# Optimization experiments

Measured on AMD Instinct MI355X. Metric: run time of the kernel, lower is better.

## Reference

```python
import jax, jax.numpy as jnp
import numpy as np

FILTER_SIZE = 7
SIGMA = 1.5
K1 = 0.01
K2 = 0.03
MAX_VAL = 1.0
CHANNEL = 1


def _gaussian_kernel3d(size, channel, sigma):
    coords = jnp.arange(size, dtype=jnp.float32) - (size - 1.0) / 2.0
    g = -(coords ** 2) / (2.0 * sigma ** 2)
    # grid[i,j,k] = g[j] + g[i] + g[k], matching torch view(1,-1,1)+view(-1,1,1)+view(1,1,-1)
    grid = g[None, :, None] + g[:, None, None] + g[None, None, :]
    grid = jax.nn.softmax(grid.reshape(-1))
    kernel = grid.reshape(1, 1, size, size, size)
    return jnp.broadcast_to(kernel, (channel, 1, size, size, size))


def _dwconv3d(x, kernel, channel):
    # depthwise (groups=channel) valid conv, NCDHW
    return jax.lax.conv_general_dilated(
        x, kernel, window_strides=(1, 1, 1), padding='VALID',
        dimension_numbers=('NCDHW', 'OIDHW', 'NCDHW'),
        feature_group_count=channel)


def setup_inputs() -> dict:
    key = jax.random.key(0)
    k1, k2 = jax.random.split(key)
    shape = (2, 1, 192, 192, 192)
    return {
        'input': jax.random.uniform(k1, shape, dtype=jnp.float32),
        'target': jax.random.uniform(k2, shape, dtype=jnp.float32),
    }


def reference(input, target):
    kernel = _gaussian_kernel3d(FILTER_SIZE, CHANNEL, SIGMA)
    c1 = (K1 * MAX_VAL) ** 2
    c2 = (K2 * MAX_VAL) ** 2
    mu1 = _dwconv3d(input, kernel, CHANNEL)
    mu2 = _dwconv3d(target, kernel, CHANNEL)
    mu1_sq = mu1 * mu1
    mu2_sq = mu2 * mu2
    mu1_mu2 = mu1 * mu2
    sigma1_sq = _dwconv3d(input * input, kernel, CHANNEL) - mu1_sq
    sigma2_sq = _dwconv3d(target * target, kernel, CHANNEL) - mu2_sq
    sigma12 = _dwconv3d(input * target, kernel, CHANNEL) - mu1_mu2
    v1 = 2.0 * sigma12 + c2
    v2 = sigma1_sq + sigma2_sq + c2
    ssim = (2.0 * mu1_mu2 + c1) * v1 / ((mu1_sq + mu2_sq + c1) * v2)
    return jnp.mean(ssim)  # reduction='mean'
```

## Files before the change

### kernel.cpp

```cpp
#include <hip/hip_runtime.h>
#include <utility>


#define DIMS 192
#define OD   186
#define VOL  (DIMS * DIMS * DIMS)
#define ZCH  62
#define XCH  27
#define NCHX 7
#define NP   (XCH + 6)
#define YT   8
#define YIN  14

#define ZP_P   15
#define ZP_F   (ZCH * ZP_P)
#define YP_F   576
#define YP_OFF (5 * ZP_F)
#define LDS_N  (YP_OFF + 5 * YP_F)

__global__ __launch_bounds__(256, 4)
void ssim3d_kernel(const float* __restrict__ X, const float* __restrict__ Y,
                   double* __restrict__ acc_out) {
    __shared__ float lds[LDS_N];
    __shared__ float wsum[4];
    const int tid = threadIdx.x;

    float w[7];
    {
        float s = 0.f;
        #pragma unroll
        for (int t = 0; t < 7; ++t) {
            float d = (float)t - 3.0f;
            w[t] = expf(-d * d / 4.5f);
            s += w[t];
        }
        #pragma unroll
        for (int t = 0; t < 7; ++t)
            w[t] = __uint_as_float(__builtin_amdgcn_readfirstlane(__float_as_uint(w[t] / s)));
    }

    const int z0 = blockIdx.x * ZCH;
    const int y0 = blockIdx.y * YT;
    const int cx = blockIdx.z % NCHX;
    const int n  = blockIdx.z / NCHX;
    const int x0 = cx * XCH;

    const float* Xb = X + (size_t)n * VOL;
    const float* Yb = Y + (size_t)n * VOL;

    const int zj = tid >> 4;
    const int zs = tid & 15;
    const bool zact = (zj < YIN);
    const int zc = z0 + zs * 4;
    const int gy = min(y0 + zj, DIMS - 1);
    const unsigned rowoff = (unsigned)gy * DIMS + (unsigned)zc;
    const bool ztail = (zc + 9 > DIMS - 1);

    const int wv = tid >> 6;
    const int ln = tid & 63;
    const int ybase = (310 * wv) >> 2;
    const int ycnt  = ((310 * (wv + 1)) >> 2) - ybase;

    const int aj = wv;
    const int ak = ln;
    const bool v1 = (ak < ZCH) && (y0 + aj < OD);
    const bool v2 = (ak < ZCH) && (y0 + aj + 4 < OD);
    const int xmax = OD + 6 - x0;

    float acc[7][10];
    #pragma unroll
    for (int q = 0; q < 7; ++q)
        #pragma unroll
        for (int m = 0; m < 10; ++m) acc[q][m] = 0.f;

    float lsum = 0.f;
    const float c1 = 1e-4f, c2 = 9e-4f;

    float pfx[10], pfy[10];

    auto loadX = [&](int xi) {
        if (!zact) return;
        int gx = min(x0 + xi, DIMS - 1);
        const float* p = Xb + (size_t)gx * (DIMS * DIMS) + rowoff;
        #pragma unroll
        for (int t = 0; t < 4; ++t) {
            float2 a = *(const float2*)(p + 2 * t);
            pfx[2 * t] = a.x; pfx[2 * t + 1] = a.y;
        }
        if (!ztail) {
            float2 a = *(const float2*)(p + 8);
            pfx[8] = a.x; pfx[9] = a.y;
        } else { pfx[8] = 0.f; pfx[9] = 0.f; }
    };
    auto loadY = [&](int xi) {
        if (!zact) return;
        int gx = min(x0 + xi, DIMS - 1);
        const float* p = Yb + (size_t)gx * (DIMS * DIMS) + rowoff;
        #pragma unroll
        for (int t = 0; t < 4; ++t) {
            float2 a = *(const float2*)(p + 2 * t);
            pfy[2 * t] = a.x; pfy[2 * t + 1] = a.y;
        }
        if (!ztail) {
            float2 a = *(const float2*)(p + 8);
            pfy[8] = a.x; pfy[9] = a.y;
        } else { pfy[8] = 0.f; pfy[9] = 0.f; }
    };

    auto ssim_pt = [&](float mu1, float mu2, float ex2, float ey2, float exy) {
        float mu11 = mu1 * mu1, mu22 = mu2 * mu2, mu12 = mu1 * mu2;
        float num = (2.f * mu12 + c1) * (2.f * (exy - mu12) + c2);
        float den = (mu11 + mu22 + c1) * ((ex2 - mu11) + (ey2 - mu22) + c2);
        lsum += num * __builtin_amdgcn_rcpf(den);
    };

    auto body = [&](int xi, auto ucell) {
        constexpr int U = decltype(ucell)::value;

        if (zact) {
            #pragma unroll
            for (int o = 0; o < 4; ++o) {
                float a0 = 0.f, a1 = 0.f, a2 = 0.f, a3 = 0.f, a4 = 0.f;
                #pragma unroll
                for (int t = 0; t < 7; ++t) {
                    float xx = pfx[o + t], yy = pfy[o + t], wt = w[t];
                    a0 += wt * xx;
                    a1 += wt * yy;
                    a2 += wt * (xx * xx);
                    a3 += wt * (yy * yy);
                    a4 += wt * (xx * yy);
                }
                int k = zs * 4 + o;
                if (k < ZCH) {
                    int b = k * ZP_P + zj;
                    lds[b]            = a0;
                    lds[b + ZP_F]     = a1;
                    lds[b + 2 * ZP_F] = a2;
                    lds[b + 3 * ZP_F] = a3;
                    lds[b + 4 * ZP_F] = a4;
                }
            }
        }
        if (xi + 1 < NP) loadX(xi + 1);
        __syncthreads();

        #pragma unroll
        for (int p2 = 0; p2 < 2; ++p2) {
            int rel = p2 * 64 + ln;
            if (rel < ycnt) {
                int t = ybase + rel;
                int f = t / ZCH;
                int k = t - f * ZCH;
                const float* src = &lds[f * ZP_F + k * ZP_P];
                float v[YIN];
                #pragma unroll
                for (int jj = 0; jj < YIN; ++jj) v[jj] = src[jj];
                float* dst = &lds[YP_OFF + f * YP_F + k * 9];
                #pragma unroll
                for (int j = 0; j < YT; ++j) {
                    float a = 0.f;
                    #pragma unroll
                    for (int tt = 0; tt < 7; ++tt) a += w[tt] * v[j + tt];
                    dst[j] = a;
                }
            }
        }
        if (xi + 1 < NP) loadY(xi + 1);
        __syncthreads();

        float vv[10];
        #pragma unroll
        for (int f = 0; f < 5; ++f) {
            vv[2 * f]     = lds[YP_OFF + f * YP_F + ak * 9 + aj];
            vv[2 * f + 1] = lds[YP_OFF + f * YP_F + ak * 9 + aj + 4];
        }
        #pragma unroll
        for (int d = 0; d < 7; ++d) {
            float wq = w[d];
            #pragma unroll
            for (int m = 0; m < 10; ++m)
                acc[(U + 7 - d) % 7][m] += wq * vv[m];
        }
        constexpr int sc = (U + 1) % 7;
        if (xi >= 6 && xi < xmax) {
            if (v1) ssim_pt(acc[sc][0], acc[sc][2], acc[sc][4], acc[sc][6], acc[sc][8]);
            if (v2) ssim_pt(acc[sc][1], acc[sc][3], acc[sc][5], acc[sc][7], acc[sc][9]);
        }
        #pragma unroll
        for (int m = 0; m < 10; ++m) acc[sc][m] = 0.f;
    };

    loadX(0); loadY(0);
    #pragma unroll 1
    for (int b = 0; b < 28; b += 7) {
        body(b + 0, std::integral_constant<int, 0>{});
        body(b + 1, std::integral_constant<int, 1>{});
        body(b + 2, std::integral_constant<int, 2>{});
        body(b + 3, std::integral_constant<int, 3>{});
        body(b + 4, std::integral_constant<int, 4>{});
        body(b + 5, std::integral_constant<int, 5>{});
        body(b + 6, std::integral_constant<int, 6>{});
    }
    body(28, std::integral_constant<int, 0>{});
    body(29, std::integral_constant<int, 1>{});
    body(30, std::integral_constant<int, 2>{});
    body(31, std::integral_constant<int, 3>{});
    body(32, std::integral_constant<int, 4>{});

    #pragma unroll
    for (int off = 32; off > 0; off >>= 1) lsum += __shfl_down(lsum, off, 64);
    if ((tid & 63) == 0) wsum[tid >> 6] = lsum;
    __syncthreads();
    if (tid == 0)
        atomicAdd(acc_out, (double)(wsum[0] + wsum[1] + wsum[2] + wsum[3]));
}

__global__ void ssim3d_finalize(const double* __restrict__ acc, float* __restrict__ out) {
    out[0] = (float)(acc[0] / 12869712.0);
}

extern "C" void kernel_launch(void* const* d_in, const int* in_sizes, int n_in,
                              void* d_out, int out_size, void* d_ws, size_t ws_size,
                              hipStream_t stream) {
    (void)in_sizes; (void)n_in; (void)out_size; (void)ws_size;
    const float* x = (const float*)d_in[0];
    const float* y = (const float*)d_in[1];
    float* out = (float*)d_out;
    double* acc = (double*)d_ws;
    hipMemsetAsync(d_ws, 0, sizeof(double), stream);
    dim3 grid(3, 24, NCHX * 2);
    ssim3d_kernel<<<grid, 256, 0, stream>>>(x, y, acc);
    ssim3d_finalize<<<1, 1, 0, stream>>>(acc, out);
}
```

Baseline: 237.8 us.

## Shrink z-tile, fuse y-pass into output stage, double-buffer LDS

The z chunk per block drops from 62 to 32, giving 6 z tiles and a larger grid, and occupancy is raised to 6 blocks per CU. The separate y-convolution pass through LDS is gone: each output thread now reads the 7 z-filtered rows directly and applies the y filter inline. The LDS tile is double-buffered so one barrier per x-step is enough, and X and Y prefetches are issued together. The global double atomic is replaced by per-block partial slots reduced by a 256-thread finalize kernel, when workspace allows. In exchange there is more redundant y-halo work per block and more LDS reads per output point.

```diff
diff --git a/kernel.cpp b/kernel.cpp
--- a/kernel.cpp
+++ b/kernel.cpp
@@ -5,22 +5,23 @@
 #define DIMS 192
 #define OD   186
 #define VOL  (DIMS * DIMS * DIMS)
-#define ZCH  62
+#define ZCH  32
+#define NZT  6
 #define XCH  27
 #define NCHX 7
 #define NP   (XCH + 6)
 #define YT   8
 #define YIN  14
-
-#define ZP_P   15
-#define ZP_F   (ZCH * ZP_P)
-#define YP_F   576
-#define YP_OFF (5 * ZP_F)
-#define LDS_N  (YP_OFF + 5 * YP_F)
-
-__global__ __launch_bounds__(256, 4)
+#define NBLK (NZT * 24 * NCHX * 2)
+
+#define ZP_J 34
+#define ZP_F (YIN * ZP_J)
+#define ZP_B (5 * ZP_F)
+#define LDS_N (2 * ZP_B)
+
+__global__ __launch_bounds__(256, 6)
 void ssim3d_kernel(const float* __restrict__ X, const float* __restrict__ Y,
-                   double* __restrict__ acc_out) {
+                   double* __restrict__ part, int use_slots) {
     __shared__ float lds[LDS_N];
     __shared__ float wsum[4];
     const int tid = threadIdx.x;
@@ -51,184 +52,179 @@
     const int zj = tid >> 4;
     const int zs = tid & 15;
     const bool zact = (zj < YIN);
-    const int zc = z0 + zs * 4;
     const int gy = min(y0 + zj, DIMS - 1);
-    const unsigned rowoff = (unsigned)gy * DIMS + (unsigned)zc;
-    const bool ztail = (zc + 9 > DIMS - 1);
-
-    const int wv = tid >> 6;
-    const int ln = tid & 63;
-    const int ybase = (310 * wv) >> 2;
-    const int ycnt  = ((310 * (wv + 1)) >> 2) - ybase;
-
-    const int aj = wv;
-    const int ak = ln;
-    const bool v1 = (ak < ZCH) && (y0 + aj < OD);
-    const bool v2 = (ak < ZCH) && (y0 + aj + 4 < OD);
-    const int xmax = OD + 6 - x0;
-
-    float acc[7][10];
+    const int zbase = z0 + 2 * zs;
+    const bool ztail = (zbase + 7 > DIMS - 1);
+    const unsigned rowoff = (unsigned)gy * DIMS + (unsigned)zbase;
+
+    const int cj = tid >> 5;
+    const int ck = tid & 31;
+    const bool cvalid = (z0 + ck < OD) && (y0 + cj < OD);
+    const int xmax = DIMS - x0;
+
+    float acc[7][5];
     #pragma unroll
     for (int q = 0; q < 7; ++q)
         #pragma unroll
-        for (int m = 0; m < 10; ++m) acc[q][m] = 0.f;
+        for (int m = 0; m < 5; ++m) acc[q][m] = 0.f;
 
     float lsum = 0.f;
     const float c1 = 1e-4f, c2 = 9e-4f;
 
-    float pfx[10], pfy[10];
+    float pfx[8], pfy[8];
 
     auto loadX = [&](int xi) {
         if (!zact) return;
         int gx = min(x0 + xi, DIMS - 1);
-        const float* p = Xb + (size_t)gx * (DIMS * DIMS) + rowoff;
-        #pragma unroll
-        for (int t = 0; t < 4; ++t) {
-            float2 a = *(const float2*)(p + 2 * t);
-            pfx[2 * t] = a.x; pfx[2 * t + 1] = a.y;
-        }
+        const float* p = Xb + (size_t)gx * (DIMS * DIMS);
         if (!ztail) {
-            float2 a = *(const float2*)(p + 8);
-            pfx[8] = a.x; pfx[9] = a.y;
-        } else { pfx[8] = 0.f; pfx[9] = 0.f; }
+            const float* q = p + rowoff;
+            #pragma unroll
+            for (int t = 0; t < 4; ++t) {
+                float2 a = *(const float2*)(q + 2 * t);
+                pfx[2 * t] = a.x; pfx[2 * t + 1] = a.y;
+            }
+        } else {
+            #pragma unroll
+            for (int t = 0; t < 8; ++t)
+                pfx[t] = p[(unsigned)gy * DIMS + (unsigned)min(zbase + t, DIMS - 1)];
+        }
     };
     auto loadY = [&](int xi) {
         if (!zact) return;
         int gx = min(x0 + xi, DIMS - 1);
-        const float* p = Yb + (size_t)gx * (DIMS * DIMS) + rowoff;
-        #pragma unroll
-        for (int t = 0; t < 4; ++t) {
-            float2 a = *(const float2*)(p + 2 * t);
-            pfy[2 * t] = a.x; pfy[2 * t + 1] = a.y;
-        }
+        const float* p = Yb + (size_t)gx * (DIMS * DIMS);
         if (!ztail) {
-            float2 a = *(const float2*)(p + 8);
-            pfy[8] = a.x; pfy[9] = a.y;
-        } else { pfy[8] = 0.f; pfy[9] = 0.f; }
+            const float* q = p + rowoff;
+            #pragma unroll
+            for (int t = 0; t < 4; ++t) {
+                float2 a = *(const float2*)(q + 2 * t);
+                pfy[2 * t] = a.x; pfy[2 * t + 1] = a.y;
+            }
+        } else {
+            #pragma unroll
+            for (int t = 0; t < 8; ++t)
+                pfy[t] = p[(unsigned)gy * DIMS + (unsigned)min(zbase + t, DIMS - 1)];
+        }
     };
 
-    auto ssim_pt = [&](float mu1, float mu2, float ex2, float ey2, float exy) {
-        float mu11 = mu1 * mu1, mu22 = mu2 * mu2, mu12 = mu1 * mu2;
-        float num = (2.f * mu12 + c1) * (2.f * (exy - mu12) + c2);
-        float den = (mu11 + mu22 + c1) * ((ex2 - mu11) + (ey2 - mu22) + c2);
-        lsum += num * __builtin_amdgcn_rcpf(den);
-    };
-
-    auto body = [&](int xi, auto ucell) {
-        constexpr int U = decltype(ucell)::value;
+    auto body = [&](int xi, auto uc, auto pc) {
+        constexpr int U = decltype(uc)::value;
+        constexpr int P = decltype(pc)::value;
+        constexpr int BUF = P * ZP_B;
 
         if (zact) {
-            #pragma unroll
-            for (int o = 0; o < 4; ++o) {
-                float a0 = 0.f, a1 = 0.f, a2 = 0.f, a3 = 0.f, a4 = 0.f;
+            float a0[2] = {0.f, 0.f}, a1[2] = {0.f, 0.f}, a2[2] = {0.f, 0.f},
+                  a3[2] = {0.f, 0.f}, a4[2] = {0.f, 0.f};
+            #pragma unroll
+            for (int t = 0; t < 7; ++t) {
+                float wt = w[t];
                 #pragma unroll
-                for (int t = 0; t < 7; ++t) {
-                    float xx = pfx[o + t], yy = pfy[o + t], wt = w[t];
-                    a0 += wt * xx;
-                    a1 += wt * yy;
-                    a2 += wt * (xx * xx);
-                    a3 += wt * (yy * yy);
-                    a4 += wt * (xx * yy);
-                }
-                int k = zs * 4 + o;
-                if (k < ZCH) {
-                    int b = k * ZP_P + zj;
-                    lds[b]            = a0;
-                    lds[b + ZP_F]     = a1;
-                    lds[b + 2 * ZP_F] = a2;
-                    lds[b + 3 * ZP_F] = a3;
-                    lds[b + 4 * ZP_F] = a4;
+                for (int o = 0; o < 2; ++o) {
+                    float xx = pfx[t + o], yy = pfy[t + o];
+                    a0[o] += wt * xx;
+                    a1[o] += wt * yy;
+                    a2[o] += wt * (xx * xx);
+                    a3[o] += wt * (yy * yy);
+                    a4[o] += wt * (xx * yy);
                 }
             }
-        }
-        if (xi + 1 < NP) loadX(xi + 1);
+            const int wb = BUF + zj * ZP_J + 2 * zs;
+            *(float2*)&lds[wb]            = make_float2(a0[0], a0[1]);
+            *(float2*)&lds[wb + ZP_F]     = make_float2(a1[0], a1[1]);
+            *(float2*)&lds[wb + 2 * ZP_F] = make_float2(a2[0], a2[1]);
+            *(float2*)&lds[wb + 3 * ZP_F] = make_float2(a3[0], a3[1]);
+            *(float2*)&lds[wb + 4 * ZP_F] = make_float2(a4[0], a4[1]);
+        }
+        if (xi + 1 < NP) { loadX(xi + 1); loadY(xi + 1); }
         __syncthreads();
 
-        #pragma unroll
-        for (int p2 = 0; p2 < 2; ++p2) {
-            int rel = p2 * 64 + ln;
-            if (rel < ycnt) {
-                int t = ybase + rel;
-                int f = t / ZCH;
-                int k = t - f * ZCH;
-                const float* src = &lds[f * ZP_F + k * ZP_P];
-                float v[YIN];
-                #pragma unroll
-                for (int jj = 0; jj < YIN; ++jj) v[jj] = src[jj];
-                float* dst = &lds[YP_OFF + f * YP_F + k * 9];
-                #pragma unroll
-                for (int j = 0; j < YT; ++j) {
-                    float a = 0.f;
-                    #pragma unroll
-                    for (int tt = 0; tt < 7; ++tt) a += w[tt] * v[j + tt];
-                    dst[j] = a;
-                }
-            }
-        }
-        if (xi + 1 < NP) loadY(xi + 1);
-        __syncthreads();
-
-        float vv[10];
+        const float* src = &lds[BUF + cj * ZP_J + ck];
+        float vv[5];
         #pragma unroll
         for (int f = 0; f < 5; ++f) {
-            vv[2 * f]     = lds[YP_OFF + f * YP_F + ak * 9 + aj];
-            vv[2 * f + 1] = lds[YP_OFF + f * YP_F + ak * 9 + aj + 4];
+            float a = 0.f;
+            #pragma unroll
+            for (int t = 0; t < 7; ++t) a += w[t] * src[f * ZP_F + t * ZP_J];
+            vv[f] = a;
         }
         #pragma unroll
         for (int d = 0; d < 7; ++d) {
             float wq = w[d];
             #pragma unroll
-            for (int m = 0; m < 10; ++m)
+            for (int m = 0; m < 5; ++m)
                 acc[(U + 7 - d) % 7][m] += wq * vv[m];
         }
         constexpr int sc = (U + 1) % 7;
-        if (xi >= 6 && xi < xmax) {
-            if (v1) ssim_pt(acc[sc][0], acc[sc][2], acc[sc][4], acc[sc][6], acc[sc][8]);
-            if (v2) ssim_pt(acc[sc][1], acc[sc][3], acc[sc][5], acc[sc][7], acc[sc][9]);
-        }
-        #pragma unroll
-        for (int m = 0; m < 10; ++m) acc[sc][m] = 0.f;
+        if (xi >= 6 && xi < xmax && cvalid) {
+            float mu1 = acc[sc][0], mu2 = acc[sc][1];
+            float ex2 = acc[sc][2], ey2 = acc[sc][3], exy = acc[sc][4];
+            float mu11 = mu1 * mu1, mu22 = mu2 * mu2, mu12 = mu1 * mu2;
+            float num = (2.f * mu12 + c1) * (2.f * (exy - mu12) + c2);
+            float den = (mu11 + mu22 + c1) * ((ex2 - mu11) + (ey2 - mu22) + c2);
+            lsum += num * __builtin_amdgcn_rcpf(den);
+        }
+        #pragma unroll
+        for (int m = 0; m < 5; ++m) acc[sc][m] = 0.f;
     };
 
     loadX(0); loadY(0);
+#define BODY(i) body(base + (i), std::integral_constant<int, (i) % 7>{}, \
+                     std::integral_constant<int, (i) % 2>{})
     #pragma unroll 1
-    for (int b = 0; b < 28; b += 7) {
-        body(b + 0, std::integral_constant<int, 0>{});
-        body(b + 1, std::integral_constant<int, 1>{});
-        body(b + 2, std::integral_constant<int, 2>{});
-        body(b + 3, std::integral_constant<int, 3>{});
-        body(b + 4, std::integral_constant<int, 4>{});
-        body(b + 5, std::integral_constant<int, 5>{});
-        body(b + 6, std::integral_constant<int, 6>{});
-    }
-    body(28, std::integral_constant<int, 0>{});
-    body(29, std::integral_constant<int, 1>{});
-    body(30, std::integral_constant<int, 2>{});
-    body(31, std::integral_constant<int, 3>{});
-    body(32, std::integral_constant<int, 4>{});
+    for (int base = 0; base < 28; base += 14) {
+        BODY(0);  BODY(1);  BODY(2);  BODY(3);  BODY(4);  BODY(5);  BODY(6);
+        BODY(7);  BODY(8);  BODY(9);  BODY(10); BODY(11); BODY(12); BODY(13);
+    }
+    {
+        const int base = 28;
+        BODY(0); BODY(1); BODY(2); BODY(3); BODY(4);
+    }
+#undef BODY
 
     #pragma unroll
     for (int off = 32; off > 0; off >>= 1) lsum += __shfl_down(lsum, off, 64);
     if ((tid & 63) == 0) wsum[tid >> 6] = lsum;
     __syncthreads();
-    if (tid == 0)
-        atomicAdd(acc_out, (double)(wsum[0] + wsum[1] + wsum[2] + wsum[3]));
+    if (tid == 0) {
+        double bs = (double)(wsum[0] + wsum[1] + wsum[2] + wsum[3]);
+        if (use_slots) {
+            int bid = blockIdx.x + NZT * (blockIdx.y + 24 * blockIdx.z);
+            part[bid] = bs;
+        } else {
+            atomicAdd(part, bs);
+        }
+    }
 }
 
-__global__ void ssim3d_finalize(const double* __restrict__ acc, float* __restrict__ out) {
-    out[0] = (float)(acc[0] / 12869712.0);
+__global__ void ssim3d_finalize(const double* __restrict__ part, float* __restrict__ out,
+                                int use_slots) {
+    __shared__ double ws[4];
+    const int tid = threadIdx.x;
+    if (!use_slots) {
+        if (tid == 0) out[0] = (float)(part[0] / 12869712.0);
+        return;
+    }
+    double s = 0.0;
+    for (int i = tid; i < NBLK; i += 256) s += part[i];
+    #pragma unroll
+    for (int off = 32; off > 0; off >>= 1) s += __shfl_down(s, off, 64);
+    if ((tid & 63) == 0) ws[tid >> 6] = s;
+    __syncthreads();
+    if (tid == 0) out[0] = (float)((ws[0] + ws[1] + ws[2] + ws[3]) / 12869712.0);
 }
 
 extern "C" void kernel_launch(void* const* d_in, const int* in_sizes, int n_in,
                               void* d_out, int out_size, void* d_ws, size_t ws_size,
                               hipStream_t stream) {
-    (void)in_sizes; (void)n_in; (void)out_size; (void)ws_size;
+    (void)in_sizes; (void)n_in; (void)out_size;
     const float* x = (const float*)d_in[0];
     const float* y = (const float*)d_in[1];
     float* out = (float*)d_out;
-    double* acc = (double*)d_ws;
-    hipMemsetAsync(d_ws, 0, sizeof(double), stream);
-    dim3 grid(3, 24, NCHX * 2);
-    ssim3d_kernel<<<grid, 256, 0, stream>>>(x, y, acc);
-    ssim3d_finalize<<<1, 1, 0, stream>>>(acc, out);
+    double* part = (double*)d_ws;
+    int use_slots = (ws_size >= NBLK * sizeof(double)) ? 1 : 0;
+    if (!use_slots) hipMemsetAsync(d_ws, 0, sizeof(double), stream);
+    dim3 grid(NZT, 24, NCHX * 2);
+    ssim3d_kernel<<<grid, 256, 0, stream>>>(x, y, part, use_slots);
+    ssim3d_finalize<<<1, 256, 0, stream>>>(part, out, use_slots);
 }
```

Measured after the change: 800.8 us. +236.8%, slower.
